# Performance work log

Hardware: AMD Instinct MI355X
Metric: run time of the kernel (lower is better)

The kernel has to match this reference:

```python
import jax, jax.numpy as jnp
import numpy as np

N_NODES = 100000
N_EDGES = 3200000
F_IN, HID, N_CLS = 256, 16, 40


def gcn_conv(x, row, col, W, b, n):
    """PyG GCNConv: x@W, symmetric deg^-1/2 normalization with self-loops, scatter-add to targets."""
    xw = x @ W  # [N, out]
    deg = jax.ops.segment_sum(jnp.ones_like(col, dtype=xw.dtype), col, num_segments=n)
    dinv = jnp.where(deg > 0, jax.lax.rsqrt(deg), jnp.zeros_like(deg))
    norm = dinv[row] * dinv[col]  # [E+N]
    out = jax.ops.segment_sum(norm[:, None] * xw[row], col, num_segments=n)
    return out + b


def setup_inputs() -> dict:
    key = jax.random.key(0)
    k1, k2, k3, k4 = jax.random.split(key, 4)
    x = jax.random.normal(k1, (N_NODES, F_IN), dtype=jnp.float32)
    edge_index = jax.random.randint(k2, (2, N_EDGES), 0, N_NODES, dtype=jnp.int64)
    W1 = jax.random.normal(k3, (F_IN, HID), dtype=jnp.float32) / np.sqrt(F_IN)
    b1 = jnp.zeros((HID,), dtype=jnp.float32)
    W2 = jax.random.normal(k4, (HID, N_CLS), dtype=jnp.float32) / np.sqrt(HID)
    b2 = jnp.zeros((N_CLS,), dtype=jnp.float32)
    return {"x": x, "edge_index": edge_index, "W1": W1, "b1": b1, "W2": W2, "b2": b2}


def reference(x, edge_index, W1, b1, W2, b2):
    n = x.shape[0]
    loop = jnp.arange(n, dtype=edge_index.dtype)
    row = jnp.concatenate([edge_index[0], loop])  # sources (+ self-loops)
    col = jnp.concatenate([edge_index[1], loop])  # targets (+ self-loops)
    h = gcn_conv(x, row, col, W1, b1, n)
    h = jax.nn.relu(h)
    # dropout p=0.5 is identity in eval mode (self.training == False)
    h = gcn_conv(h, row, col, W2, b2, n)
    return jax.nn.log_softmax(h, axis=1)
```

## Files before the change

### kernel.cpp

```cpp
#include <hip/hip_runtime.h>

#define F_IN 256
#define HID  16
#define NCLS 40
#define NB   512
#define CAP  18944
#define SPAN 8192

static inline int cdiv(int a, int b) { return (a + b - 1) / b; }

typedef short bf16x8 __attribute__((ext_vector_type(8)));
typedef float f32x4  __attribute__((ext_vector_type(4)));

__device__ __forceinline__ float bf_lo(unsigned int u) { return __uint_as_float(u << 16); }
__device__ __forceinline__ float bf_hi(unsigned int u) { return __uint_as_float(u & 0xFFFF0000u); }
__device__ __forceinline__ unsigned short f2bf(float a) {
    unsigned int u = __float_as_uint(a);
    return (unsigned short)((u + 0x7FFFu + ((u >> 16) & 1u)) >> 16);
}
__device__ __forceinline__ unsigned int pack_bf(float a, float b) {
    return (unsigned int)f2bf(a) | ((unsigned int)f2bf(b) << 16);
}

__global__ void __launch_bounds__(256) bcount_kernel(const int* __restrict__ col,
                                                     int* __restrict__ bkt_cnt, int E, int K) {
    __shared__ int h[256];
    int t = threadIdx.x;
    h[t] = 0;
    __syncthreads();
    int E4 = E >> 2;
    const int4* c4 = (const int4*)col;
    for (int e = blockIdx.x * 256 + t; e < E4; e += gridDim.x * 256) {
        int4 v = c4[e];
        atomicAdd(&h[v.x >> 9], 1);
        atomicAdd(&h[v.y >> 9], 1);
        atomicAdd(&h[v.z >> 9], 1);
        atomicAdd(&h[v.w >> 9], 1);
    }
    for (int e = (E4 << 2) + blockIdx.x * 256 + t; e < E; e += gridDim.x * 256)
        atomicAdd(&h[col[e] >> 9], 1);
    __syncthreads();
    if (t < K && h[t]) atomicAdd(&bkt_cnt[t], h[t]);
}

__global__ void __launch_bounds__(256) bscan_kernel(const int* __restrict__ bkt_cnt,
                                                    int* __restrict__ bkt_off,
                                                    int* __restrict__ bkt_cur, int K) {
    __shared__ int s[256];
    int t = threadIdx.x;
    int v = (t < K) ? bkt_cnt[t] : 0;
    s[t] = v;
    __syncthreads();
    for (int off = 1; off < 256; off <<= 1) {
        int x = (t >= off) ? s[t - off] : 0;
        __syncthreads();
        s[t] += x;
        __syncthreads();
    }
    int excl = s[t] - v;
    if (t < K) { bkt_off[t] = excl; bkt_cur[t] = excl; }
    if (t == K - 1) bkt_off[K] = excl + v;
}

__global__ void __launch_bounds__(256) bscatter_kernel(const int* __restrict__ row,
                                                       const int* __restrict__ col,
                                                       int* __restrict__ bkt_cur,
                                                       int* __restrict__ entries, int E) {
    __shared__ int cnt[256];
    __shared__ int base[256];
    int t = threadIdx.x;
    int start = blockIdx.x * SPAN;
    int end = min(start + SPAN, E);
    cnt[t] = 0;
    __syncthreads();
    int m = end - start;
    int m4 = m >> 2;
    const int4* c4 = (const int4*)(col + start);
    for (int i = t; i < m4; i += 256) {
        int4 v = c4[i];
        atomicAdd(&cnt[v.x >> 9], 1);
        atomicAdd(&cnt[v.y >> 9], 1);
        atomicAdd(&cnt[v.z >> 9], 1);
        atomicAdd(&cnt[v.w >> 9], 1);
    }
    for (int i = (m4 << 2) + t; i < m; i += 256)
        atomicAdd(&cnt[col[start + i] >> 9], 1);
    __syncthreads();
    int c = cnt[t];
    base[t] = c ? atomicAdd(&bkt_cur[t], c) : 0;
    cnt[t] = 0;
    __syncthreads();
    for (int e = start + t; e < end; e += 256) {
        int cc = col[e];
        int bkt = cc >> 9;
        int pos = base[bkt] + atomicAdd(&cnt[bkt], 1);
        entries[pos] = row[e] | ((cc & (NB - 1)) << 17);
    }
}

__global__ void __launch_bounds__(512) bfill_kernel(const int* __restrict__ entries,
                                                    const int* __restrict__ bkt_off,
                                                    int* __restrict__ csr_src,
                                                    int* __restrict__ csr_off,
                                                    float* __restrict__ dinv, int n, int E) {
    __shared__ int sdeg[NB];
    __shared__ int soff[NB];
    __shared__ int wtot[8];
    __shared__ int lsrc[CAP];
    int t = threadIdx.x;
    int wv = t >> 6, ln = t & 63;
    int b = blockIdx.x;
    int node0 = b << 9;
    int nn = min(NB, n - node0);
    int seg0 = bkt_off[b], seg1 = bkt_off[b + 1];
    int m = seg1 - seg0;
    sdeg[t] = 0;
    __syncthreads();
    for (int i = t; i < m; i += 512) atomicAdd(&sdeg[entries[seg0 + i] >> 17], 1);
    __syncthreads();
    int v = sdeg[t];
    int inc = v;
#pragma unroll
    for (int o = 1; o < 64; o <<= 1) {
        int u = __shfl_up(inc, o);
        if (ln >= o) inc += u;
    }
    if (ln == 63) wtot[wv] = inc;
    __syncthreads();
    if (wv == 0) {
        int tv = (ln < 8) ? wtot[ln] : 0;
        int ti = tv;
#pragma unroll
        for (int o = 1; o < 8; o <<= 1) {
            int u = __shfl_up(ti, o);
            if (ln >= o) ti += u;
        }
        if (ln < 8) wtot[ln] = ti - tv;
    }
    __syncthreads();
    int excl = inc - v + wtot[wv];
    sdeg[t] = 0;
    soff[t] = excl;
    __syncthreads();
    for (int i = t; i < m; i += 512) {
        int u = entries[seg0 + i];
        int l = u >> 17;
        int pos = soff[l] + atomicAdd(&sdeg[l], 1);
        lsrc[pos] = u & 0x1FFFF;
    }
    __syncthreads();
    for (int i = t; i < m; i += 512) csr_src[seg0 + i] = lsrc[i];
    if (t < nn) {
        csr_off[node0 + t] = seg0 + excl;
        dinv[node0 + t] = rsqrtf((float)(v + 1));
    }
    if (b == gridDim.x - 1 && t == 0) csr_off[n] = E;
}

__global__ void __launch_bounds__(256) xw_kernel(const float* __restrict__ x,
                                                 const float* __restrict__ W1,
                                                 const float* __restrict__ dinv,
                                                 unsigned short* __restrict__ f1,
                                                 int ntiles) {
    int lane = threadIdx.x & 63;
    int m = lane & 15;
    int q = lane >> 4;
    bf16x8 bfrag[8];
#pragma unroll
    for (int c = 0; c < 8; ++c) {
        const float* wp = W1 + (size_t)(c * 32 + q * 8) * HID + m;
#pragma unroll
        for (int j = 0; j < 8; ++j) bfrag[c][j] = (short)f2bf(wp[(size_t)j * HID]);
    }
    int wid = (blockIdx.x * 256 + threadIdx.x) >> 6;
    if (wid >= ntiles) return;
    int r0 = wid << 4;
    const float* xrow = x + (size_t)(r0 + m) * F_IN + q * 8;
    f32x4 acc = {0.f, 0.f, 0.f, 0.f};
#pragma unroll
    for (int c = 0; c < 8; ++c) {
        float4 v0 = *(const float4*)(xrow + c * 32);
        float4 v1 = *(const float4*)(xrow + c * 32 + 4);
        bf16x8 afrag;
        afrag[0] = (short)f2bf(v0.x);
        afrag[1] = (short)f2bf(v0.y);
        afrag[2] = (short)f2bf(v0.z);
        afrag[3] = (short)f2bf(v0.w);
        afrag[4] = (short)f2bf(v1.x);
        afrag[5] = (short)f2bf(v1.y);
        afrag[6] = (short)f2bf(v1.z);
        afrag[7] = (short)f2bf(v1.w);
        acc = __builtin_amdgcn_mfma_f32_16x16x32_bf16(afrag, bfrag[c], acc, 0, 0, 0);
    }
#pragma unroll
    for (int i = 0; i < 4; ++i) {
        int r = r0 + q * 4 + i;
        f1[(size_t)r * HID + m] = f2bf(dinv[r] * acc[i]);
    }
}

__global__ void __launch_bounds__(256) agg1_kernel(const unsigned int* __restrict__ feat,
                                                   const float* __restrict__ dinv,
                                                   const int* __restrict__ csr_off,
                                                   const int* __restrict__ csr_src,
                                                   const float* __restrict__ b1,
                                                   unsigned int* __restrict__ f2, int n) {
    int wid = (blockIdx.x * 256 + threadIdx.x) >> 6;
    if (wid >= n) return;
    int lane = threadIdx.x & 63;
    int j = lane & 7, s = lane >> 3;
    int start = csr_off[wid], end = csr_off[wid + 1];
    float a0 = 0.f, a1 = 0.f;
    int ei = start + s;
    for (; ei + 24 < end; ei += 32) {
        int i0 = csr_src[ei];
        int i1 = csr_src[ei + 8];
        int i2 = csr_src[ei + 16];
        int i3 = csr_src[ei + 24];
        unsigned int u0 = feat[(size_t)i0 * 8 + j];
        unsigned int u1 = feat[(size_t)i1 * 8 + j];
        unsigned int u2 = feat[(size_t)i2 * 8 + j];
        unsigned int u3 = feat[(size_t)i3 * 8 + j];
        a0 += bf_lo(u0); a1 += bf_hi(u0);
        a0 += bf_lo(u1); a1 += bf_hi(u1);
        a0 += bf_lo(u2); a1 += bf_hi(u2);
        a0 += bf_lo(u3); a1 += bf_hi(u3);
    }
    for (; ei < end; ei += 8) {
        unsigned int u = feat[(size_t)csr_src[ei] * 8 + j];
        a0 += bf_lo(u); a1 += bf_hi(u);
    }
    a0 += __shfl_xor(a0, 8);  a1 += __shfl_xor(a1, 8);
    a0 += __shfl_xor(a0, 16); a1 += __shfl_xor(a1, 16);
    a0 += __shfl_xor(a0, 32); a1 += __shfl_xor(a1, 32);
    if (lane < 8) {
        unsigned int us = feat[(size_t)wid * 8 + j];
        float dc = dinv[wid];
        float v0 = fmaxf(dc * (a0 + bf_lo(us)) + b1[2 * j],     0.f);
        float v1 = fmaxf(dc * (a1 + bf_hi(us)) + b1[2 * j + 1], 0.f);
        f2[(size_t)wid * 8 + j] = pack_bf(dc * v0, dc * v1);
    }
}

__global__ void __launch_bounds__(256) agg2out_kernel(const unsigned int* __restrict__ feat,
                                                      const float* __restrict__ dinv,
                                                      const int* __restrict__ csr_off,
                                                      const int* __restrict__ csr_src,
                                                      const float* __restrict__ W2,
                                                      const float* __restrict__ b2,
                                                      float* __restrict__ out, int n) {
    __shared__ float W2s[HID * NCLS];
    __shared__ float b2s[NCLS];
    for (int i = threadIdx.x; i < HID * NCLS; i += 256) W2s[i] = W2[i];
    if (threadIdx.x < NCLS) b2s[threadIdx.x] = b2[threadIdx.x];
    __syncthreads();
    int wid = (blockIdx.x * 256 + threadIdx.x) >> 6;
    if (wid >= n) return;
    int lane = threadIdx.x & 63;
    int j = lane & 7, s = lane >> 3;
    int start = csr_off[wid], end = csr_off[wid + 1];
    float a0 = 0.f, a1 = 0.f;
    int ei = start + s;
    for (; ei + 24 < end; ei += 32) {
        int i0 = csr_src[ei];
        int i1 = csr_src[ei + 8];
        int i2 = csr_src[ei + 16];
        int i3 = csr_src[ei + 24];
        unsigned int u0 = feat[(size_t)i0 * 8 + j];
        unsigned int u1 = feat[(size_t)i1 * 8 + j];
        unsigned int u2 = feat[(size_t)i2 * 8 + j];
        unsigned int u3 = feat[(size_t)i3 * 8 + j];
        a0 += bf_lo(u0); a1 += bf_hi(u0);
        a0 += bf_lo(u1); a1 += bf_hi(u1);
        a0 += bf_lo(u2); a1 += bf_hi(u2);
        a0 += bf_lo(u3); a1 += bf_hi(u3);
    }
    for (; ei < end; ei += 8) {
        unsigned int u = feat[(size_t)csr_src[ei] * 8 + j];
        a0 += bf_lo(u); a1 += bf_hi(u);
    }
    if (s == 0) {
        unsigned int us = feat[(size_t)wid * 8 + j];
        a0 += bf_lo(us); a1 += bf_hi(us);
    }
    a0 += __shfl_xor(a0, 8);  a1 += __shfl_xor(a1, 8);
    a0 += __shfl_xor(a0, 16); a1 += __shfl_xor(a1, 16);
    a0 += __shfl_xor(a0, 32); a1 += __shfl_xor(a1, 32);
    float dc = dinv[wid];
    float z = (lane < NCLS) ? b2s[lane] : 0.f;
#pragma unroll
    for (int q = 0; q < 8; ++q) {
        float e0 = dc * __shfl(a0, q);
        float e1 = dc * __shfl(a1, q);
        if (lane < NCLS) {
            z += e0 * W2s[(2 * q)     * NCLS + lane];
            z += e1 * W2s[(2 * q + 1) * NCLS + lane];
        }
    }
    float zz = (lane < NCLS) ? z : -INFINITY;
#pragma unroll
    for (int off = 1; off < 64; off <<= 1) zz = fmaxf(zz, __shfl_xor(zz, off));
    float es = (lane < NCLS) ? __expf(z - zz) : 0.f;
#pragma unroll
    for (int off = 1; off < 64; off <<= 1) es += __shfl_xor(es, off);
    float lse = zz + __logf(es);
    if (lane < NCLS) out[(size_t)wid * NCLS + lane] = z - lse;
}

extern "C" void kernel_launch(void* const* d_in, const int* in_sizes, int n_in,
                              void* d_out, int out_size, void* d_ws, size_t ws_size,
                              hipStream_t stream) {
    const float* x   = (const float*)d_in[0];
    const int*   ei  = (const int*)d_in[1];
    const float* W1  = (const float*)d_in[2];
    const float* b1  = (const float*)d_in[3];
    const float* W2  = (const float*)d_in[4];
    const float* b2  = (const float*)d_in[5];
    float*       out = (float*)d_out;

    int n = in_sizes[0] / F_IN;
    int E = in_sizes[1] / 2;
    const int* rowp = ei;
    const int* colp = ei + E;
    int K = cdiv(n, NB);

    char* p = (char*)d_ws;
    auto alloc = [&](size_t bytes) {
        char* q = p;
        p += (bytes + 255) & ~(size_t)255;
        return q;
    };
    int*   bkt_cnt = (int*)  alloc((size_t)K * 4);
    int*   bkt_off = (int*)  alloc(((size_t)K + 1) * 4);
    int*   bkt_cur = (int*)  alloc((size_t)K * 4);
    int*   csr_off = (int*)  alloc(((size_t)n + 1) * 4);
    int*   csr_src = (int*)  alloc((size_t)E * 4);
    float* dinv    = (float*)alloc((size_t)n * 4);
    size_t fbytes = (size_t)n * HID * 2;
    char* region = alloc((size_t)E * 4 > 2 * fbytes ? (size_t)E * 4 : 2 * fbytes);
    int*            entries = (int*)region;
    unsigned short* f1      = (unsigned short*)region;
    unsigned int*   f2      = (unsigned int*)(region + fbytes);

    hipMemsetAsync(bkt_cnt, 0, (size_t)K * 4, stream);
    bcount_kernel<<<1024, 256, 0, stream>>>(colp, bkt_cnt, E, K);
    bscan_kernel<<<1, 256, 0, stream>>>(bkt_cnt, bkt_off, bkt_cur, K);
    bscatter_kernel<<<cdiv(E, SPAN), 256, 0, stream>>>(rowp, colp, bkt_cur, entries, E);
    bfill_kernel<<<K, 512, 0, stream>>>(entries, bkt_off, csr_src, csr_off, dinv, n, E);

    int ntiles = n >> 4;
    xw_kernel<<<cdiv(ntiles, 4), 256, 0, stream>>>(x, W1, dinv, f1, ntiles);
    agg1_kernel<<<cdiv(n, 4), 256, 0, stream>>>((const unsigned int*)f1, dinv, csr_off, csr_src, b1, f2, n);
    agg2out_kernel<<<cdiv(n, 4), 256, 0, stream>>>(f2, dinv, csr_off, csr_src, W2, b2, out, n);
}
```

Measured before the change: 374.0 us.

## Aggregate two nodes per wavefront in both GCN aggregation kernels

Each 64-lane wavefront now handles two destination nodes: each half-wave of 32 lanes processes one node's edges using 4 edge slots times 8 feature lanes, instead of one node per wave with 8 edge slots. With an average degree of about 32, this is meant to cut idle lanes and per-wave overhead and to halve the wave count. The second kernel computes the W2 projection and log-softmax for both nodes with interleaved shuffles. The trade-off is fewer edges in flight per node and a doubled epilogue per wave.

```diff
diff --git a/kernel.cpp b/kernel.cpp
--- a/kernel.cpp
+++ b/kernel.cpp
@@ -206,39 +206,52 @@
                                                    const float* __restrict__ b1,
                                                    unsigned int* __restrict__ f2, int n) {
     int wid = (blockIdx.x * 256 + threadIdx.x) >> 6;
-    if (wid >= n) return;
+    int w0 = wid << 1;
+    if (w0 >= n) return;
     int lane = threadIdx.x & 63;
-    int j = lane & 7, s = lane >> 3;
-    int start = csr_off[wid], end = csr_off[wid + 1];
-    float a0 = 0.f, a1 = 0.f;
-    int ei = start + s;
-    for (; ei + 24 < end; ei += 32) {
+    int j = lane & 7;
+    int node = w0 + (lane >> 5);
+    int s4 = (lane >> 3) & 3;
+    bool act = node < n;
+    int start = 0, end = 0;
+    if (act) { start = csr_off[node]; end = csr_off[node + 1]; }
+    float r0 = 0.f, r1 = 0.f;
+    int ei = start + s4;
+    for (; ei + 12 < end; ei += 16) {
         int i0 = csr_src[ei];
-        int i1 = csr_src[ei + 8];
-        int i2 = csr_src[ei + 16];
-        int i3 = csr_src[ei + 24];
+        int i1 = csr_src[ei + 4];
+        int i2 = csr_src[ei + 8];
+        int i3 = csr_src[ei + 12];
         unsigned int u0 = feat[(size_t)i0 * 8 + j];
         unsigned int u1 = feat[(size_t)i1 * 8 + j];
         unsigned int u2 = feat[(size_t)i2 * 8 + j];
         unsigned int u3 = feat[(size_t)i3 * 8 + j];
-        a0 += bf_lo(u0); a1 += bf_hi(u0);
-        a0 += bf_lo(u1); a1 += bf_hi(u1);
-        a0 += bf_lo(u2); a1 += bf_hi(u2);
-        a0 += bf_lo(u3); a1 += bf_hi(u3);
-    }
-    for (; ei < end; ei += 8) {
+        r0 += bf_lo(u0); r1 += bf_hi(u0);
+        r0 += bf_lo(u1); r1 += bf_hi(u1);
+        r0 += bf_lo(u2); r1 += bf_hi(u2);
+        r0 += bf_lo(u3); r1 += bf_hi(u3);
+    }
+    for (; ei < end; ei += 4) {
         unsigned int u = feat[(size_t)csr_src[ei] * 8 + j];
-        a0 += bf_lo(u); a1 += bf_hi(u);
-    }
-    a0 += __shfl_xor(a0, 8);  a1 += __shfl_xor(a1, 8);
-    a0 += __shfl_xor(a0, 16); a1 += __shfl_xor(a1, 16);
-    a0 += __shfl_xor(a0, 32); a1 += __shfl_xor(a1, 32);
-    if (lane < 8) {
-        unsigned int us = feat[(size_t)wid * 8 + j];
-        float dc = dinv[wid];
-        float v0 = fmaxf(dc * (a0 + bf_lo(us)) + b1[2 * j],     0.f);
-        float v1 = fmaxf(dc * (a1 + bf_hi(us)) + b1[2 * j + 1], 0.f);
-        f2[(size_t)wid * 8 + j] = pack_bf(dc * v0, dc * v1);
+        r0 += bf_lo(u); r1 += bf_hi(u);
+    }
+    if (act && s4 == 0) {
+        unsigned int us = feat[(size_t)node * 8 + j];
+        r0 += bf_lo(us); r1 += bf_hi(us);
+    }
+    r0 += __shfl_xor(r0, 8);  r1 += __shfl_xor(r1, 8);
+    r0 += __shfl_xor(r0, 16); r1 += __shfl_xor(r1, 16);
+    float x0 = __shfl_xor(r0, 32), x1 = __shfl_xor(r1, 32);
+    if (lane < 16) {
+        int wsel = w0 + (lane >> 3);
+        if (wsel < n) {
+            float s0 = (lane < 8) ? r0 : x0;
+            float s1 = (lane < 8) ? r1 : x1;
+            float dc = dinv[wsel];
+            float v0 = fmaxf(dc * s0 + b1[2 * j],     0.f);
+            float v1 = fmaxf(dc * s1 + b1[2 * j + 1], 0.f);
+            f2[(size_t)w0 * 8 + lane] = pack_bf(dc * v0, dc * v1);
+        }
     }
 }
 
@@ -255,56 +268,84 @@
     if (threadIdx.x < NCLS) b2s[threadIdx.x] = b2[threadIdx.x];
     __syncthreads();
     int wid = (blockIdx.x * 256 + threadIdx.x) >> 6;
-    if (wid >= n) return;
+    int w0 = wid << 1;
+    if (w0 >= n) return;
     int lane = threadIdx.x & 63;
-    int j = lane & 7, s = lane >> 3;
-    int start = csr_off[wid], end = csr_off[wid + 1];
-    float a0 = 0.f, a1 = 0.f;
-    int ei = start + s;
-    for (; ei + 24 < end; ei += 32) {
+    int j = lane & 7;
+    int node = w0 + (lane >> 5);
+    int s4 = (lane >> 3) & 3;
+    bool act = node < n;
+    int start = 0, end = 0;
+    if (act) { start = csr_off[node]; end = csr_off[node + 1]; }
+    float r0 = 0.f, r1 = 0.f;
+    int ei = start + s4;
+    for (; ei + 12 < end; ei += 16) {
         int i0 = csr_src[ei];
-        int i1 = csr_src[ei + 8];
-        int i2 = csr_src[ei + 16];
-        int i3 = csr_src[ei + 24];
+        int i1 = csr_src[ei + 4];
+        int i2 = csr_src[ei + 8];
+        int i3 = csr_src[ei + 12];
         unsigned int u0 = feat[(size_t)i0 * 8 + j];
         unsigned int u1 = feat[(size_t)i1 * 8 + j];
         unsigned int u2 = feat[(size_t)i2 * 8 + j];
         unsigned int u3 = feat[(size_t)i3 * 8 + j];
-        a0 += bf_lo(u0); a1 += bf_hi(u0);
-        a0 += bf_lo(u1); a1 += bf_hi(u1);
-        a0 += bf_lo(u2); a1 += bf_hi(u2);
-        a0 += bf_lo(u3); a1 += bf_hi(u3);
-    }
-    for (; ei < end; ei += 8) {
+        r0 += bf_lo(u0); r1 += bf_hi(u0);
+        r0 += bf_lo(u1); r1 += bf_hi(u1);
+        r0 += bf_lo(u2); r1 += bf_hi(u2);
+        r0 += bf_lo(u3); r1 += bf_hi(u3);
+    }
+    for (; ei < end; ei += 4) {
         unsigned int u = feat[(size_t)csr_src[ei] * 8 + j];
-        a0 += bf_lo(u); a1 += bf_hi(u);
-    }
-    if (s == 0) {
-        unsigned int us = feat[(size_t)wid * 8 + j];
-        a0 += bf_lo(us); a1 += bf_hi(us);
-    }
-    a0 += __shfl_xor(a0, 8);  a1 += __shfl_xor(a1, 8);
-    a0 += __shfl_xor(a0, 16); a1 += __shfl_xor(a1, 16);
-    a0 += __shfl_xor(a0, 32); a1 += __shfl_xor(a1, 32);
-    float dc = dinv[wid];
-    float z = (lane < NCLS) ? b2s[lane] : 0.f;
+        r0 += bf_lo(u); r1 += bf_hi(u);
+    }
+    if (act && s4 == 0) {
+        unsigned int us = feat[(size_t)node * 8 + j];
+        r0 += bf_lo(us); r1 += bf_hi(us);
+    }
+    r0 += __shfl_xor(r0, 8);  r1 += __shfl_xor(r1, 8);
+    r0 += __shfl_xor(r0, 16); r1 += __shfl_xor(r1, 16);
+    float x0 = __shfl_xor(r0, 32), x1 = __shfl_xor(r1, 32);
+    float a0 = (lane < 32) ? r0 : x0;
+    float a1 = (lane < 32) ? r1 : x1;
+    float c0 = (lane < 32) ? x0 : r0;
+    float c1 = (lane < 32) ? x1 : r1;
+    bool hasB = (w0 + 1) < n;
+    float dcA = dinv[w0];
+    float dcB = hasB ? dinv[w0 + 1] : 0.f;
+    float zA = (lane < NCLS) ? b2s[lane] : 0.f;
+    float zB = zA;
 #pragma unroll
     for (int q = 0; q < 8; ++q) {
-        float e0 = dc * __shfl(a0, q);
-        float e1 = dc * __shfl(a1, q);
+        float e0A = dcA * __shfl(a0, q);
+        float e1A = dcA * __shfl(a1, q);
+        float e0B = dcB * __shfl(c0, q);
+        float e1B = dcB * __shfl(c1, q);
         if (lane < NCLS) {
-            z += e0 * W2s[(2 * q)     * NCLS + lane];
-            z += e1 * W2s[(2 * q + 1) * NCLS + lane];
+            float w0v = W2s[(2 * q)     * NCLS + lane];
+            float w1v = W2s[(2 * q + 1) * NCLS + lane];
+            zA += e0A * w0v + e1A * w1v;
+            zB += e0B * w0v + e1B * w1v;
         }
     }
-    float zz = (lane < NCLS) ? z : -INFINITY;
-#pragma unroll
-    for (int off = 1; off < 64; off <<= 1) zz = fmaxf(zz, __shfl_xor(zz, off));
-    float es = (lane < NCLS) ? __expf(z - zz) : 0.f;
-#pragma unroll
-    for (int off = 1; off < 64; off <<= 1) es += __shfl_xor(es, off);
-    float lse = zz + __logf(es);
-    if (lane < NCLS) out[(size_t)wid * NCLS + lane] = z - lse;
+    float mA = (lane < NCLS) ? zA : -INFINITY;
+    float mB = (lane < NCLS) ? zB : -INFINITY;
+#pragma unroll
+    for (int off = 1; off < 64; off <<= 1) {
+        mA = fmaxf(mA, __shfl_xor(mA, off));
+        mB = fmaxf(mB, __shfl_xor(mB, off));
+    }
+    float eA = (lane < NCLS) ? __expf(zA - mA) : 0.f;
+    float eB = (lane < NCLS) ? __expf(zB - mB) : 0.f;
+#pragma unroll
+    for (int off = 1; off < 64; off <<= 1) {
+        eA += __shfl_xor(eA, off);
+        eB += __shfl_xor(eB, off);
+    }
+    float lseA = mA + __logf(eA);
+    float lseB = mB + __logf(eB);
+    if (lane < NCLS) {
+        out[(size_t)w0 * NCLS + lane] = zA - lseA;
+        if (hasB) out[(size_t)(w0 + 1) * NCLS + lane] = zB - lseB;
+    }
 }
 
 extern "C" void kernel_launch(void* const* d_in, const int* in_sizes, int n_in,
@@ -350,6 +391,7 @@
 
     int ntiles = n >> 4;
     xw_kernel<<<cdiv(ntiles, 4), 256, 0, stream>>>(x, W1, dinv, f1, ntiles);
-    agg1_kernel<<<cdiv(n, 4), 256, 0, stream>>>((const unsigned int*)f1, dinv, csr_off, csr_src, b1, f2, n);
-    agg2out_kernel<<<cdiv(n, 4), 256, 0, stream>>>(f2, dinv, csr_off, csr_src, W2, b2, out, n);
-}
+    int npair = cdiv(n, 2);
+    agg1_kernel<<<cdiv(npair, 4), 256, 0, stream>>>((const unsigned int*)f1, dinv, csr_off, csr_src, b1, f2, n);
+    agg2out_kernel<<<cdiv(npair, 4), 256, 0, stream>>>(f2, dinv, csr_off, csr_src, W2, b2, out, n);
+}
```

Measured after the change: 358.7 us. 1.04x faster.
